# Kernel optimization log

Hardware: AMD Instinct MI355X
Metric: run time of the kernel (lower is better)

The kernel has to match this reference:

```python
import jax, jax.numpy as jnp
import numpy as np

MASK_WEIGHT = 1.0
HEAD_DIM = 64
SCALING = HEAD_DIM ** -0.5


def _rotate_half(x):
    x1, x2 = jnp.split(x, 2, axis=-1)
    return jnp.concatenate([-x2, x1], axis=-1)


def _rope_tables(seq_len, dim, dtype):
    inv_freq = 1.0 / (10000.0 ** (jnp.arange(0, dim, 2, dtype=jnp.float32) / dim))
    t = jnp.arange(seq_len, dtype=jnp.float32)
    freqs = jnp.outer(t, inv_freq)                      # (s, d/2)
    cos = jnp.tile(jnp.cos(freqs), (1, 2)).astype(dtype)  # (s, d)  '(2 d)' tiling
    sin = jnp.tile(jnp.sin(freqs), (1, 2)).astype(dtype)
    return cos, sin


def _apply_rope(x, cos, sin):
    # x: (b, h, s, d); cos/sin: (s, d) broadcast over b, h
    return x * cos + _rotate_half(x) * sin


def setup_inputs() -> dict:
    key = jax.random.key(0)
    ks = jax.random.split(key, 6)
    b, h, s, d = 2, 16, 2048, 64
    d_model = h * d
    return {
        "q": jax.random.normal(ks[0], (b, h, s, d), jnp.float32),
        "k": jax.random.normal(ks[1], (b, h, s, d), jnp.float32),
        "v": jax.random.normal(ks[2], (b, h, s, d), jnp.float32),
        "attention_mask": jax.random.normal(ks[3], (1, h, s, s), jnp.float32) * 0.05,
        "out_w": jax.random.normal(ks[4], (d_model, d_model), jnp.float32) * (d_model ** -0.5),
        "out_b": jax.random.normal(ks[5], (d_model,), jnp.float32) * 0.02,
    }


def reference(q, k, v, attention_mask, out_w, out_b):
    b, h, s, d = q.shape
    cos, sin = _rope_tables(s, d, q.dtype)
    qr = _apply_rope(q, cos, sin)
    kr = _apply_rope(k, cos, sin)
    # learned per-head affinity transform of the queries: q' = (mask_weight * W) @ q
    W = attention_mask[0] * MASK_WEIGHT                    # (h, s, s), shared over batch
    qt = jnp.einsum('hqk,bhkd->bhqd', W, qr)
    # flash-style online softmax over keys == plain stable softmax (same math)
    scores = jnp.einsum('bhqd,bhkd->bhqk', qt, kr) * SCALING
    attn = jax.nn.softmax(scores, axis=-1)
    ctx = jnp.einsum('bhqk,bhkd->bhqd', attn, v)
    ctx = ctx.transpose(0, 2, 1, 3).reshape(b, s, h * d)   # (b, s, d_model)
    return ctx @ out_w.T + out_b
```

## Files before the change

### kernel.cpp

```cpp
#include <hip/hip_runtime.h>
#include <hip/hip_bf16.h>
#include <math.h>

typedef __bf16 bf16_t;
typedef __bf16 bf16x4 __attribute__((ext_vector_type(4)));
typedef __bf16 bf16x8 __attribute__((ext_vector_type(8)));
typedef float f32x4 __attribute__((ext_vector_type(4)));

#define NB 2
#define NH 16
#define SEQ 2048
#define HD 64
#define DMODEL 1024
#define QK_SCALE 0.125f
#define LOG2E 1.44269504088896340f
#define INV_2PI 0.15915494309189535f

__device__ __forceinline__ bf16_t to_bf16(float x) { return (bf16_t)x; }
#define MFMA16 __builtin_amdgcn_mfma_f32_16x16x32_bf16

__global__ __launch_bounds__(256) void k1_rope_pack(
    const float* __restrict__ q, const float* __restrict__ k, const float* __restrict__ v,
    bf16_t* __restrict__ qrT, bf16_t* __restrict__ krN, bf16_t* __restrict__ vT)
{
  __shared__ bf16_t tile[64][65];
  const int tid = threadIdx.x;
  const int blk = blockIdx.x;
  const int st = blk & 31;
  const int bh = blk >> 5;
  const int s0 = st * 64;

  const size_t base_sd = ((size_t)bh * SEQ + s0) * HD;
  const float* qb = q + base_sd;
  const float* kb = k + base_sd;
  const float* vb = v + base_sd;
  bf16_t* qrTb = qrT + (size_t)bh * HD * SEQ;
  bf16_t* krNb = krN + base_sd;
  bf16_t* vTb  = vT  + (size_t)bh * HD * SEQ;

  #pragma unroll
  for (int pp = 0; pp < 2; ++pp) {
    int idx = pp * 256 + tid;
    int sr = idx >> 3;
    int j0 = (idx & 7) * 4;
    float4 q1 = *(const float4*)&qb[sr*HD + j0];
    float4 q2 = *(const float4*)&qb[sr*HD + j0 + 32];
    float4 ka = *(const float4*)&kb[sr*HD + j0];
    float4 kc = *(const float4*)&kb[sr*HD + j0 + 32];
    float q1a[4] = {q1.x, q1.y, q1.z, q1.w};
    float q2a[4] = {q2.x, q2.y, q2.z, q2.w};
    float kaa[4] = {ka.x, ka.y, ka.z, ka.w};
    float kca[4] = {kc.x, kc.y, kc.z, kc.w};
    bf16x4 kr1, kr2;
    #pragma unroll
    for (int t = 0; t < 4; ++t) {
      int j = j0 + t;
      float freq = __builtin_amdgcn_exp2f(-(float)j * (13.287712379549449f / 32.0f));
      float ang = (float)(s0 + sr) * freq;
      float rev = ang * INV_2PI;
      rev = rev - floorf(rev);
      float c  = __builtin_amdgcn_cosf(rev);
      float sn = __builtin_amdgcn_sinf(rev);
      tile[sr][j]      = to_bf16((q1a[t]*c - q2a[t]*sn) * QK_SCALE);
      tile[sr][j + 32] = to_bf16((q2a[t]*c + q1a[t]*sn) * QK_SCALE);
      kr1[t] = to_bf16(kaa[t]*c - kca[t]*sn);
      kr2[t] = to_bf16(kca[t]*c + kaa[t]*sn);
    }
    *(bf16x4*)&krNb[sr*HD + j0]      = kr1;
    *(bf16x4*)&krNb[sr*HD + j0 + 32] = kr2;
  }
  __syncthreads();
  #pragma unroll
  for (int c = 0; c < 2; ++c) {
    int id = c*256 + tid;
    int d = id >> 3;
    int sc = (id & 7) * 8;
    bf16x8 vec;
    #pragma unroll
    for (int i = 0; i < 8; ++i) vec[i] = tile[sc + i][d];
    *(bf16x8*)&qrTb[(size_t)d * SEQ + s0 + sc] = vec;
  }
  __syncthreads();
  #pragma unroll
  for (int c = 0; c < 4; ++c) {
    int id = c*256 + tid;
    int sr = id >> 4;
    int c4 = (id & 15) * 4;
    float4 v4 = *(const float4*)&vb[sr*HD + c4];
    tile[sr][c4+0] = to_bf16(v4.x);
    tile[sr][c4+1] = to_bf16(v4.y);
    tile[sr][c4+2] = to_bf16(v4.z);
    tile[sr][c4+3] = to_bf16(v4.w);
  }
  __syncthreads();
  #pragma unroll
  for (int c = 0; c < 2; ++c) {
    int id = c*256 + tid;
    int d = id >> 3;
    int sc = (id & 7) * 8;
    bf16x8 vec;
    #pragma unroll
    for (int i = 0; i < 8; ++i) vec[i] = tile[sc + i][d];
    *(bf16x8*)&vTb[(size_t)d * SEQ + s0 + sc] = vec;
  }
}

__global__ __launch_bounds__(256) void k2_qt_gemm(
    const float* __restrict__ Wm,
    const bf16_t* __restrict__ qrT,
    bf16_t* __restrict__ qtT)
{
  __shared__ __align__(16) bf16_t A_lds[2][64*72];
  __shared__ __align__(16) bf16_t B_lds[64*72];
  const int tid = threadIdx.x;
  const int blk = (blockIdx.x & 7) * 64 + (blockIdx.x >> 3);
  const int n0 = (blk & 31) * 64;
  const int h = blk >> 5;
  const int wave = tid >> 6, lane = tid & 63;
  const int l15 = lane & 15, quad = lane >> 4;
  const int rs = tid >> 2, cs = (tid & 3) * 16;

  const float* Wh = Wm + (size_t)h * SEQ * SEQ + (size_t)n0 * SEQ;
  const bf16_t* A0 = qrT + ((size_t)h * HD + rs) * SEQ;
  const bf16_t* A1 = qrT + (((size_t)NH + h) * HD + rs) * SEQ;

  f32x4 acc[2][4] = {};
  float4 wreg[4];
  bf16x8 areg[2][2];

  #pragma unroll
  for (int i = 0; i < 4; ++i) wreg[i] = *(const float4*)&Wh[(size_t)rs*SEQ + cs + i*4];
  #pragma unroll
  for (int i = 0; i < 2; ++i) {
    areg[0][i] = *(const bf16x8*)&A0[cs + i*8];
    areg[1][i] = *(const bf16x8*)&A1[cs + i*8];
  }

  for (int it = 0; it < SEQ/64; ++it) {
    if (it) __syncthreads();
    #pragma unroll
    for (int i = 0; i < 2; ++i) {
      *(bf16x8*)&A_lds[0][rs*72 + cs + i*8] = areg[0][i];
      *(bf16x8*)&A_lds[1][rs*72 + cs + i*8] = areg[1][i];
      bf16x8 wb;
      float4 wa = wreg[i*2], wc = wreg[i*2+1];
      wb[0]=to_bf16(wa.x); wb[1]=to_bf16(wa.y); wb[2]=to_bf16(wa.z); wb[3]=to_bf16(wa.w);
      wb[4]=to_bf16(wc.x); wb[5]=to_bf16(wc.y); wb[6]=to_bf16(wc.z); wb[7]=to_bf16(wc.w);
      *(bf16x8*)&B_lds[rs*72 + cs + i*8] = wb;
    }
    __syncthreads();
    if (it + 1 < SEQ/64) {
      int kb = (it + 1) * 64;
      #pragma unroll
      for (int i = 0; i < 4; ++i) wreg[i] = *(const float4*)&Wh[(size_t)rs*SEQ + kb + cs + i*4];
      #pragma unroll
      for (int i = 0; i < 2; ++i) {
        areg[0][i] = *(const bf16x8*)&A0[kb + cs + i*8];
        areg[1][i] = *(const bf16x8*)&A1[kb + cs + i*8];
      }
    }
    #pragma unroll
    for (int kc = 0; kc < 2; ++kc) {
      const int off = kc*32 + quad*8;
      bf16x8 bfr[4];
      #pragma unroll
      for (int nt = 0; nt < 4; ++nt)
        bfr[nt] = *(const bf16x8*)&B_lds[(nt*16 + l15)*72 + off];
      #pragma unroll
      for (int b2 = 0; b2 < 2; ++b2) {
        bf16x8 af = *(const bf16x8*)&A_lds[b2][(wave*16 + l15)*72 + off];
        #pragma unroll
        for (int nt = 0; nt < 4; ++nt)
          acc[b2][nt] = MFMA16(af, bfr[nt], acc[b2][nt], 0, 0, 0);
      }
    }
  }
  #pragma unroll
  for (int b2 = 0; b2 < 2; ++b2)
    #pragma unroll
    for (int nt = 0; nt < 4; ++nt)
      #pragma unroll
      for (int r = 0; r < 4; ++r) {
        int d = wave*16 + quad*4 + r;
        qtT[(((size_t)b2*NH + h)*HD + d)*SEQ + n0 + nt*16 + l15] =
            to_bf16(acc[b2][nt][r] * LOG2E);
      }
}

__global__ __launch_bounds__(256, 2) void k3_flash(
    const bf16_t* __restrict__ qtT,
    const bf16_t* __restrict__ krN,
    const bf16_t* __restrict__ vT,
    bf16_t* __restrict__ ctx)
{
  __shared__ __align__(16) bf16_t K_lds[64*72];
  __shared__ __align__(16) bf16_t V_lds[64*72];
  __shared__ __align__(16) bf16_t P_lds[4][16*72];
  const int tid = threadIdx.x;
  const int blk = (blockIdx.x & 7) * 64 + (blockIdx.x >> 3);
  const int qt = blk & 15;
  const int bh = blk >> 4;
  const int h = bh & 15, b = bh >> 4;
  const int wave = tid >> 6, lane = tid & 63;
  const int l15 = lane & 15, quad = lane >> 4;
  const int qw = qt*128 + wave*32;
  const int srow = tid >> 3, sch = (tid & 7) * 8;

  const bf16_t* qtb = qtT + (size_t)bh * HD * SEQ;
  const bf16_t* krb = krN + (size_t)bh * SEQ * HD;
  const bf16_t* vtb = vT  + (size_t)bh * HD * SEQ;

  bf16x8 Qf[2][2];
  #pragma unroll
  for (int g = 0; g < 2; ++g)
    #pragma unroll
    for (int c = 0; c < 2; ++c)
      #pragma unroll
      for (int j = 0; j < 8; ++j)
        Qf[g][c][j] = qtb[(size_t)(c*32 + quad*8 + j)*SEQ + qw + g*16 + l15];

  bf16x8 ones;
  #pragma unroll
  for (int j = 0; j < 8; ++j) ones[j] = to_bf16(1.0f);

  f32x4 O[2][4] = {};
  f32x4 L[2] = {};

  bf16x8 kreg[2], vreg[2];
  #pragma unroll
  for (int c = 0; c < 2; ++c) {
    int row = c*32 + srow;
    kreg[c] = *(const bf16x8*)&krb[(size_t)row*HD + sch];
    vreg[c] = *(const bf16x8*)&vtb[(size_t)row*SEQ + sch];
  }

  for (int kt = 0; kt < 32; ++kt) {
    if (kt) __syncthreads();
    #pragma unroll
    for (int c = 0; c < 2; ++c) {
      int row = c*32 + srow;
      *(bf16x8*)&K_lds[row*72 + sch] = kreg[c];
      *(bf16x8*)&V_lds[row*72 + sch] = vreg[c];
    }
    __syncthreads();
    if (kt + 1 < 32) {
      #pragma unroll
      for (int c = 0; c < 2; ++c) {
        int row = c*32 + srow;
        kreg[c] = *(const bf16x8*)&krb[(size_t)((kt+1)*64 + row)*HD + sch];
        vreg[c] = *(const bf16x8*)&vtb[(size_t)row*SEQ + (kt+1)*64 + sch];
      }
    }

    bf16x8 ak[4][2], bv[4][2];
    #pragma unroll
    for (int nt = 0; nt < 4; ++nt) {
      ak[nt][0] = *(const bf16x8*)&K_lds[(nt*16 + l15)*72 + quad*8];
      ak[nt][1] = *(const bf16x8*)&K_lds[(nt*16 + l15)*72 + 32 + quad*8];
      bv[nt][0] = *(const bf16x8*)&V_lds[(nt*16 + l15)*72 + quad*8];
      bv[nt][1] = *(const bf16x8*)&V_lds[(nt*16 + l15)*72 + 32 + quad*8];
    }

    #pragma unroll
    for (int g = 0; g < 2; ++g) {
      f32x4 s[4] = {};
      __builtin_amdgcn_s_setprio(1);
      #pragma unroll
      for (int nt = 0; nt < 4; ++nt) {
        s[nt] = MFMA16(ak[nt][0], Qf[g][0], s[nt], 0, 0, 0);
        s[nt] = MFMA16(ak[nt][1], Qf[g][1], s[nt], 0, 0, 0);
      }
      __builtin_amdgcn_s_setprio(0);
      #pragma unroll
      for (int nt = 0; nt < 4; ++nt) {
        bf16x4 pk;
        #pragma unroll
        for (int r = 0; r < 4; ++r)
          pk[r] = to_bf16(__builtin_amdgcn_exp2f(s[nt][r]));
        *(bf16x4*)&P_lds[wave][l15*72 + nt*16 + quad*4] = pk;
      }
      bf16x8 ap0 = *(const bf16x8*)&P_lds[wave][l15*72 + quad*8];
      bf16x8 ap1 = *(const bf16x8*)&P_lds[wave][l15*72 + 32 + quad*8];
      __builtin_amdgcn_s_setprio(1);
      #pragma unroll
      for (int nt = 0; nt < 4; ++nt) {
        O[g][nt] = MFMA16(ap0, bv[nt][0], O[g][nt], 0, 0, 0);
        O[g][nt] = MFMA16(ap1, bv[nt][1], O[g][nt], 0, 0, 0);
      }
      L[g] = MFMA16(ap0, ones, L[g], 0, 0, 0);
      L[g] = MFMA16(ap1, ones, L[g], 0, 0, 0);
      __builtin_amdgcn_s_setprio(0);
    }
  }

  #pragma unroll
  for (int g = 0; g < 2; ++g)
    #pragma unroll
    for (int nt = 0; nt < 4; ++nt)
      #pragma unroll
      for (int r = 0; r < 4; ++r) {
        int qrow = qw + g*16 + quad*4 + r;
        float o = O[g][nt][r] / L[g][r];
        ctx[((size_t)b*SEQ + qrow)*DMODEL + h*HD + nt*16 + l15] = to_bf16(o);
      }
}

__global__ __launch_bounds__(256) void k4_proj(
    const bf16_t* __restrict__ ctx,
    const float* __restrict__ w,
    const float* __restrict__ bias,
    float* __restrict__ out)
{
  __shared__ __align__(16) bf16_t A_lds[128*72];
  __shared__ __align__(16) bf16_t B_lds[64*72];
  const int tid = threadIdx.x;
  const int blk = blockIdx.x;
  const int n0 = (blk & 15) * 64;
  const int m0 = (blk >> 4) * 128;
  const int wave = tid >> 6, lane = tid & 63;
  const int l15 = lane & 15, quad = lane >> 4;
  const int ra = tid >> 1, ca = (tid & 1) * 32;
  const int rs = tid >> 2, cs = (tid & 3) * 16;

  f32x4 acc[2][4] = {};
  bf16x8 areg[4];
  float4 wreg[4];

  #pragma unroll
  for (int i = 0; i < 4; ++i) {
    areg[i] = *(const bf16x8*)&ctx[(size_t)(m0 + ra)*DMODEL + ca + i*8];
    wreg[i] = *(const float4*)&w[(size_t)(n0 + rs)*DMODEL + cs + i*4];
  }

  for (int it = 0; it < DMODEL/64; ++it) {
    if (it) __syncthreads();
    #pragma unroll
    for (int i = 0; i < 4; ++i)
      *(bf16x8*)&A_lds[ra*72 + ca + i*8] = areg[i];
    #pragma unroll
    for (int i = 0; i < 2; ++i) {
      bf16x8 wb;
      float4 wa = wreg[i*2], wc = wreg[i*2+1];
      wb[0]=to_bf16(wa.x); wb[1]=to_bf16(wa.y); wb[2]=to_bf16(wa.z); wb[3]=to_bf16(wa.w);
      wb[4]=to_bf16(wc.x); wb[5]=to_bf16(wc.y); wb[6]=to_bf16(wc.z); wb[7]=to_bf16(wc.w);
      *(bf16x8*)&B_lds[rs*72 + cs + i*8] = wb;
    }
    __syncthreads();
    if (it + 1 < DMODEL/64) {
      int kb = (it + 1) * 64;
      #pragma unroll
      for (int i = 0; i < 4; ++i) {
        areg[i] = *(const bf16x8*)&ctx[(size_t)(m0 + ra)*DMODEL + kb + ca + i*8];
        wreg[i] = *(const float4*)&w[(size_t)(n0 + rs)*DMODEL + kb + cs + i*4];
      }
    }
    #pragma unroll
    for (int kc = 0; kc < 2; ++kc) {
      const int off = kc*32 + quad*8;
      bf16x8 bfr[4];
      #pragma unroll
      for (int nt = 0; nt < 4; ++nt)
        bfr[nt] = *(const bf16x8*)&B_lds[(nt*16 + l15)*72 + off];
      #pragma unroll
      for (int g = 0; g < 2; ++g) {
        bf16x8 af = *(const bf16x8*)&A_lds[(wave*32 + g*16 + l15)*72 + off];
        #pragma unroll
        for (int nt = 0; nt < 4; ++nt)
          acc[g][nt] = MFMA16(af, bfr[nt], acc[g][nt], 0, 0, 0);
      }
    }
  }
  #pragma unroll
  for (int nt = 0; nt < 4; ++nt) {
    float bb = bias[n0 + nt*16 + l15];
    #pragma unroll
    for (int g = 0; g < 2; ++g)
      #pragma unroll
      for (int r = 0; r < 4; ++r)
        out[(size_t)(m0 + wave*32 + g*16 + quad*4 + r)*DMODEL + n0 + nt*16 + l15] =
            acc[g][nt][r] + bb;
  }
}

extern "C" void kernel_launch(void* const* d_in, const int* in_sizes, int n_in,
                              void* d_out, int out_size, void* d_ws, size_t ws_size,
                              hipStream_t stream)
{
  const float* q     = (const float*)d_in[0];
  const float* k     = (const float*)d_in[1];
  const float* v     = (const float*)d_in[2];
  const float* mask  = (const float*)d_in[3];
  const float* out_w = (const float*)d_in[4];
  const float* out_b = (const float*)d_in[5];
  float* out = (float*)d_out;

  const size_t elems = (size_t)NB * NH * SEQ * HD;
  bf16_t* qrT = (bf16_t*)d_ws;
  bf16_t* krN = qrT + elems;
  bf16_t* vT  = krN + elems;
  bf16_t* qtT = vT  + elems;
  bf16_t* ctx = qtT + elems;

  k1_rope_pack<<<dim3(NB*NH*(SEQ/64)), dim3(256), 0, stream>>>(q, k, v, qrT, krN, vT);
  k2_qt_gemm <<<dim3(NH*(SEQ/64)),     dim3(256), 0, stream>>>(mask, qrT, qtT);
  k3_flash   <<<dim3(NB*NH*(SEQ/128)), dim3(256), 0, stream>>>(qtT, krN, vT, ctx);
  k4_proj    <<<dim3((NB*SEQ/128)*(DMODEL/64)), dim3(256), 0, stream>>>(ctx, out_w, out_b, out);
}
```

Baseline: 492.9 us.

## Load K/V fragments directly from global into registers with double buffering

The flash kernel no longer stages K and V tiles through shared memory with block-wide barriers. Each wave now loads its MFMA operand fragments straight from global memory into two register buffers, prefetching the next tile while the current one is computed. This removes the LDS round trip and both __syncthreads per tile. In exchange, each of the four waves reads the same K/V data from global/L2 separately, which is four times the global traffic, and the extra register buffers raise register pressure and may reduce occupancy.

```diff
diff --git a/kernel.cpp b/kernel.cpp
--- a/kernel.cpp
+++ b/kernel.cpp
@@ -193,8 +193,6 @@
     const bf16_t* __restrict__ vT,
     bf16_t* __restrict__ ctx)
 {
-  __shared__ __align__(16) bf16_t K_lds[64*72];
-  __shared__ __align__(16) bf16_t V_lds[64*72];
   __shared__ __align__(16) bf16_t P_lds[4][16*72];
   const int tid = threadIdx.x;
   const int blk = (blockIdx.x & 7) * 64 + (blockIdx.x >> 3);
@@ -204,11 +202,10 @@
   const int wave = tid >> 6, lane = tid & 63;
   const int l15 = lane & 15, quad = lane >> 4;
   const int qw = qt*128 + wave*32;
-  const int srow = tid >> 3, sch = (tid & 7) * 8;
 
   const bf16_t* qtb = qtT + (size_t)bh * HD * SEQ;
-  const bf16_t* krb = krN + (size_t)bh * SEQ * HD;
-  const bf16_t* vtb = vT  + (size_t)bh * HD * SEQ;
+  const bf16_t* krb = krN + (size_t)bh * SEQ * HD + (size_t)l15 * HD + quad*8;
+  const bf16_t* vtb = vT  + (size_t)bh * HD * SEQ + (size_t)l15 * SEQ + quad*8;
 
   bf16x8 Qf[2][2];
   #pragma unroll
@@ -226,72 +223,63 @@
   f32x4 O[2][4] = {};
   f32x4 L[2] = {};
 
-  bf16x8 kreg[2], vreg[2];
-  #pragma unroll
-  for (int c = 0; c < 2; ++c) {
-    int row = c*32 + srow;
-    kreg[c] = *(const bf16x8*)&krb[(size_t)row*HD + sch];
-    vreg[c] = *(const bf16x8*)&vtb[(size_t)row*SEQ + sch];
-  }
-
-  for (int kt = 0; kt < 32; ++kt) {
-    if (kt) __syncthreads();
-    #pragma unroll
-    for (int c = 0; c < 2; ++c) {
-      int row = c*32 + srow;
-      *(bf16x8*)&K_lds[row*72 + sch] = kreg[c];
-      *(bf16x8*)&V_lds[row*72 + sch] = vreg[c];
-    }
-    __syncthreads();
-    if (kt + 1 < 32) {
-      #pragma unroll
-      for (int c = 0; c < 2; ++c) {
-        int row = c*32 + srow;
-        kreg[c] = *(const bf16x8*)&krb[(size_t)((kt+1)*64 + row)*HD + sch];
-        vreg[c] = *(const bf16x8*)&vtb[(size_t)row*SEQ + (kt+1)*64 + sch];
-      }
-    }
-
-    bf16x8 ak[4][2], bv[4][2];
-    #pragma unroll
-    for (int nt = 0; nt < 4; ++nt) {
-      ak[nt][0] = *(const bf16x8*)&K_lds[(nt*16 + l15)*72 + quad*8];
-      ak[nt][1] = *(const bf16x8*)&K_lds[(nt*16 + l15)*72 + 32 + quad*8];
-      bv[nt][0] = *(const bf16x8*)&V_lds[(nt*16 + l15)*72 + quad*8];
-      bv[nt][1] = *(const bf16x8*)&V_lds[(nt*16 + l15)*72 + 32 + quad*8];
-    }
-
-    #pragma unroll
-    for (int g = 0; g < 2; ++g) {
-      f32x4 s[4] = {};
-      __builtin_amdgcn_s_setprio(1);
-      #pragma unroll
-      for (int nt = 0; nt < 4; ++nt) {
-        s[nt] = MFMA16(ak[nt][0], Qf[g][0], s[nt], 0, 0, 0);
-        s[nt] = MFMA16(ak[nt][1], Qf[g][1], s[nt], 0, 0, 0);
-      }
-      __builtin_amdgcn_s_setprio(0);
-      #pragma unroll
-      for (int nt = 0; nt < 4; ++nt) {
-        bf16x4 pk;
-        #pragma unroll
-        for (int r = 0; r < 4; ++r)
-          pk[r] = to_bf16(__builtin_amdgcn_exp2f(s[nt][r]));
-        *(bf16x4*)&P_lds[wave][l15*72 + nt*16 + quad*4] = pk;
-      }
-      bf16x8 ap0 = *(const bf16x8*)&P_lds[wave][l15*72 + quad*8];
-      bf16x8 ap1 = *(const bf16x8*)&P_lds[wave][l15*72 + 32 + quad*8];
-      __builtin_amdgcn_s_setprio(1);
-      #pragma unroll
-      for (int nt = 0; nt < 4; ++nt) {
-        O[g][nt] = MFMA16(ap0, bv[nt][0], O[g][nt], 0, 0, 0);
-        O[g][nt] = MFMA16(ap1, bv[nt][1], O[g][nt], 0, 0, 0);
-      }
-      L[g] = MFMA16(ap0, ones, L[g], 0, 0, 0);
-      L[g] = MFMA16(ap1, ones, L[g], 0, 0, 0);
-      __builtin_amdgcn_s_setprio(0);
-    }
-  }
+  bf16x8 akA[4][2], bvA[4][2], akB[4][2], bvB[4][2];
+
+#define LOADT(AK, BV, KT) do {                                            \
+    const bf16_t* kp_ = krb + (size_t)(KT) * 64 * HD;                     \
+    const bf16_t* vp_ = vtb + (size_t)(KT) * 64;                          \
+    _Pragma("unroll")                                                     \
+    for (int nt_ = 0; nt_ < 4; ++nt_) {                                   \
+      _Pragma("unroll")                                                   \
+      for (int c_ = 0; c_ < 2; ++c_) {                                    \
+        AK[nt_][c_] = *(const bf16x8*)&kp_[nt_*16*HD + c_*32];            \
+        BV[nt_][c_] = *(const bf16x8*)&vp_[(size_t)nt_*16*SEQ + c_*32];   \
+      }                                                                   \
+    }                                                                     \
+  } while (0)
+
+#define COMPUTE(AK, BV) do {                                              \
+    _Pragma("unroll")                                                     \
+    for (int g = 0; g < 2; ++g) {                                         \
+      f32x4 s_[4] = {};                                                   \
+      __builtin_amdgcn_s_setprio(1);                                      \
+      _Pragma("unroll")                                                   \
+      for (int nt = 0; nt < 4; ++nt) {                                    \
+        s_[nt] = MFMA16(AK[nt][0], Qf[g][0], s_[nt], 0, 0, 0);            \
+        s_[nt] = MFMA16(AK[nt][1], Qf[g][1], s_[nt], 0, 0, 0);            \
+      }                                                                   \
+      __builtin_amdgcn_s_setprio(0);                                      \
+      _Pragma("unroll")                                                   \
+      for (int nt = 0; nt < 4; ++nt) {                                    \
+        bf16x4 pk;                                                        \
+        _Pragma("unroll")                                                 \
+        for (int r = 0; r < 4; ++r)                                       \
+          pk[r] = to_bf16(__builtin_amdgcn_exp2f(s_[nt][r]));             \
+        *(bf16x4*)&P_lds[wave][l15*72 + nt*16 + quad*4] = pk;             \
+      }                                                                   \
+      bf16x8 ap0 = *(const bf16x8*)&P_lds[wave][l15*72 + quad*8];         \
+      bf16x8 ap1 = *(const bf16x8*)&P_lds[wave][l15*72 + 32 + quad*8];    \
+      __builtin_amdgcn_s_setprio(1);                                      \
+      _Pragma("unroll")                                                   \
+      for (int nt = 0; nt < 4; ++nt) {                                    \
+        O[g][nt] = MFMA16(ap0, BV[nt][0], O[g][nt], 0, 0, 0);             \
+        O[g][nt] = MFMA16(ap1, BV[nt][1], O[g][nt], 0, 0, 0);             \
+      }                                                                   \
+      L[g] = MFMA16(ap0, ones, L[g], 0, 0, 0);                            \
+      L[g] = MFMA16(ap1, ones, L[g], 0, 0, 0);                            \
+      __builtin_amdgcn_s_setprio(0);                                      \
+    }                                                                     \
+  } while (0)
+
+  LOADT(akA, bvA, 0);
+  for (int kt = 0; kt < 32; kt += 2) {
+    LOADT(akB, bvB, kt + 1);
+    COMPUTE(akA, bvA);
+    if (kt + 2 < 32) LOADT(akA, bvA, kt + 2);
+    COMPUTE(akB, bvB);
+  }
+#undef LOADT
+#undef COMPUTE
 
   #pragma unroll
   for (int g = 0; g < 2; ++g)
```

New measurement: 562.4 us. 1.14x slower.

## Halve flash query tile per block and raise occupancy to four blocks

Applied to the files above, without the earlier changes.

The flash attention kernel now handles 64 queries per block (16 per wave) instead of 128, doubling the grid to 1024 blocks, and launch bounds request 4 blocks per CU. K/V fragments are read from LDS inside the MFMA loops instead of being preloaded into registers. This lowers register pressure so more waves can hide latency, but each K/V tile loaded into LDS is reused by half as many queries, doubling global K/V traffic and the LDS fill work.

```diff
diff --git a/kernel.cpp b/kernel.cpp
--- a/kernel.cpp
+++ b/kernel.cpp
@@ -187,7 +187,7 @@
       }
 }
 
-__global__ __launch_bounds__(256, 2) void k3_flash(
+__global__ __launch_bounds__(256, 4) void k3_flash(
     const bf16_t* __restrict__ qtT,
     const bf16_t* __restrict__ krN,
     const bf16_t* __restrict__ vT,
@@ -197,34 +197,32 @@
   __shared__ __align__(16) bf16_t V_lds[64*72];
   __shared__ __align__(16) bf16_t P_lds[4][16*72];
   const int tid = threadIdx.x;
-  const int blk = (blockIdx.x & 7) * 64 + (blockIdx.x >> 3);
-  const int qt = blk & 15;
-  const int bh = blk >> 4;
+  const int blk = (blockIdx.x & 7) * 128 + (blockIdx.x >> 3);
+  const int qt = blk & 31;
+  const int bh = blk >> 5;
   const int h = bh & 15, b = bh >> 4;
   const int wave = tid >> 6, lane = tid & 63;
   const int l15 = lane & 15, quad = lane >> 4;
-  const int qw = qt*128 + wave*32;
+  const int qw = qt*64 + wave*16;
   const int srow = tid >> 3, sch = (tid & 7) * 8;
 
   const bf16_t* qtb = qtT + (size_t)bh * HD * SEQ;
   const bf16_t* krb = krN + (size_t)bh * SEQ * HD;
   const bf16_t* vtb = vT  + (size_t)bh * HD * SEQ;
 
-  bf16x8 Qf[2][2];
-  #pragma unroll
-  for (int g = 0; g < 2; ++g)
-    #pragma unroll
-    for (int c = 0; c < 2; ++c)
-      #pragma unroll
-      for (int j = 0; j < 8; ++j)
-        Qf[g][c][j] = qtb[(size_t)(c*32 + quad*8 + j)*SEQ + qw + g*16 + l15];
+  bf16x8 Qf[2];
+  #pragma unroll
+  for (int c = 0; c < 2; ++c)
+    #pragma unroll
+    for (int j = 0; j < 8; ++j)
+      Qf[c][j] = qtb[(size_t)(c*32 + quad*8 + j)*SEQ + qw + l15];
 
   bf16x8 ones;
   #pragma unroll
   for (int j = 0; j < 8; ++j) ones[j] = to_bf16(1.0f);
 
-  f32x4 O[2][4] = {};
-  f32x4 L[2] = {};
+  f32x4 O[4] = {};
+  f32x4 L = {};
 
   bf16x8 kreg[2], vreg[2];
   #pragma unroll
@@ -252,57 +250,48 @@
       }
     }
 
-    bf16x8 ak[4][2], bv[4][2];
+    f32x4 s[4];
+    __builtin_amdgcn_s_setprio(1);
     #pragma unroll
     for (int nt = 0; nt < 4; ++nt) {
-      ak[nt][0] = *(const bf16x8*)&K_lds[(nt*16 + l15)*72 + quad*8];
-      ak[nt][1] = *(const bf16x8*)&K_lds[(nt*16 + l15)*72 + 32 + quad*8];
-      bv[nt][0] = *(const bf16x8*)&V_lds[(nt*16 + l15)*72 + quad*8];
-      bv[nt][1] = *(const bf16x8*)&V_lds[(nt*16 + l15)*72 + 32 + quad*8];
-    }
-
-    #pragma unroll
-    for (int g = 0; g < 2; ++g) {
-      f32x4 s[4] = {};
-      __builtin_amdgcn_s_setprio(1);
-      #pragma unroll
-      for (int nt = 0; nt < 4; ++nt) {
-        s[nt] = MFMA16(ak[nt][0], Qf[g][0], s[nt], 0, 0, 0);
-        s[nt] = MFMA16(ak[nt][1], Qf[g][1], s[nt], 0, 0, 0);
-      }
-      __builtin_amdgcn_s_setprio(0);
-      #pragma unroll
-      for (int nt = 0; nt < 4; ++nt) {
-        bf16x4 pk;
-        #pragma unroll
-        for (int r = 0; r < 4; ++r)
-          pk[r] = to_bf16(__builtin_amdgcn_exp2f(s[nt][r]));
-        *(bf16x4*)&P_lds[wave][l15*72 + nt*16 + quad*4] = pk;
-      }
-      bf16x8 ap0 = *(const bf16x8*)&P_lds[wave][l15*72 + quad*8];
-      bf16x8 ap1 = *(const bf16x8*)&P_lds[wave][l15*72 + 32 + quad*8];
-      __builtin_amdgcn_s_setprio(1);
-      #pragma unroll
-      for (int nt = 0; nt < 4; ++nt) {
-        O[g][nt] = MFMA16(ap0, bv[nt][0], O[g][nt], 0, 0, 0);
-        O[g][nt] = MFMA16(ap1, bv[nt][1], O[g][nt], 0, 0, 0);
-      }
-      L[g] = MFMA16(ap0, ones, L[g], 0, 0, 0);
-      L[g] = MFMA16(ap1, ones, L[g], 0, 0, 0);
-      __builtin_amdgcn_s_setprio(0);
-    }
-  }
-
-  #pragma unroll
-  for (int g = 0; g < 2; ++g)
-    #pragma unroll
-    for (int nt = 0; nt < 4; ++nt)
-      #pragma unroll
-      for (int r = 0; r < 4; ++r) {
-        int qrow = qw + g*16 + quad*4 + r;
-        float o = O[g][nt][r] / L[g][r];
-        ctx[((size_t)b*SEQ + qrow)*DMODEL + h*HD + nt*16 + l15] = to_bf16(o);
-      }
+      bf16x8 ak0 = *(const bf16x8*)&K_lds[(nt*16 + l15)*72 + quad*8];
+      bf16x8 ak1 = *(const bf16x8*)&K_lds[(nt*16 + l15)*72 + 32 + quad*8];
+      f32x4 z = {};
+      z = MFMA16(ak0, Qf[0], z, 0, 0, 0);
+      s[nt] = MFMA16(ak1, Qf[1], z, 0, 0, 0);
+    }
+    __builtin_amdgcn_s_setprio(0);
+    #pragma unroll
+    for (int nt = 0; nt < 4; ++nt) {
+      bf16x4 pk;
+      #pragma unroll
+      for (int r = 0; r < 4; ++r)
+        pk[r] = to_bf16(__builtin_amdgcn_exp2f(s[nt][r]));
+      *(bf16x4*)&P_lds[wave][l15*72 + nt*16 + quad*4] = pk;
+    }
+    bf16x8 ap0 = *(const bf16x8*)&P_lds[wave][l15*72 + quad*8];
+    bf16x8 ap1 = *(const bf16x8*)&P_lds[wave][l15*72 + 32 + quad*8];
+    __builtin_amdgcn_s_setprio(1);
+    #pragma unroll
+    for (int nt = 0; nt < 4; ++nt) {
+      bf16x8 bv0 = *(const bf16x8*)&V_lds[(nt*16 + l15)*72 + quad*8];
+      bf16x8 bv1 = *(const bf16x8*)&V_lds[(nt*16 + l15)*72 + 32 + quad*8];
+      O[nt] = MFMA16(ap0, bv0, O[nt], 0, 0, 0);
+      O[nt] = MFMA16(ap1, bv1, O[nt], 0, 0, 0);
+    }
+    L = MFMA16(ap0, ones, L, 0, 0, 0);
+    L = MFMA16(ap1, ones, L, 0, 0, 0);
+    __builtin_amdgcn_s_setprio(0);
+  }
+
+  #pragma unroll
+  for (int nt = 0; nt < 4; ++nt)
+    #pragma unroll
+    for (int r = 0; r < 4; ++r) {
+      int qrow = qw + quad*4 + r;
+      float o = O[nt][r] / L[r];
+      ctx[((size_t)b*SEQ + qrow)*DMODEL + h*HD + nt*16 + l15] = to_bf16(o);
+    }
 }
 
 __global__ __launch_bounds__(256) void k4_proj(
@@ -403,6 +392,6 @@
 
   k1_rope_pack<<<dim3(NB*NH*(SEQ/64)), dim3(256), 0, stream>>>(q, k, v, qrT, krN, vT);
   k2_qt_gemm <<<dim3(NH*(SEQ/64)),     dim3(256), 0, stream>>>(mask, qrT, qtT);
-  k3_flash   <<<dim3(NB*NH*(SEQ/128)), dim3(256), 0, stream>>>(qtT, krN, vT, ctx);
+  k3_flash   <<<dim3(NB*NH*(SEQ/64)),  dim3(256), 0, stream>>>(qtT, krN, vT, ctx);
   k4_proj    <<<dim3((NB*SEQ/128)*(DMODEL/64)), dim3(256), 0, stream>>>(ctx, out_w, out_b, out);
 }
```

Measured after the change: 501.7 us. No clear change (+1.8%).
